# Kernel optimization log

Measured on AMD Instinct MI355X. Metric: run time of the kernel, lower is better.

The kernel has to match this reference:

```python
import jax, jax.numpy as jnp
import numpy as np
from jax import lax

B, C, N, T, K = 16, 64, 512, 64, 3
EPS = 1e-5


def _bn(x, g, b):
    # training-mode BatchNorm2d over (B, H=N, W=T) per channel
    m = jnp.mean(x, axis=(0, 2, 3), keepdims=True)
    v = jnp.var(x, axis=(0, 2, 3), keepdims=True)
    return (x - m) * lax.rsqrt(v + EPS) * g[None, :, None, None] + b[None, :, None, None]


def _conv(x, w, b, pad):
    y = lax.conv_general_dilated(x, w, (1, 1), ((0, 0), pad),
                                 dimension_numbers=('NCHW', 'OIHW', 'NCHW'))
    return y + b[None, :, None, None]


def setup_inputs() -> dict:
    key = jax.random.key(0)
    ks = jax.random.split(key, 8)
    xav = lambda k, sh, fi, fo: jax.random.normal(k, sh, jnp.float32) * np.sqrt(2.0 / (fi + fo))
    return {
        'x': jax.random.normal(ks[0], (B, C, N, T), jnp.float32),
        'adj_mx': jax.random.normal(ks[1], (K, N, N), jnp.float32) / np.sqrt(N),
        'cheb_w': xav(ks[2], (K, C, C), C, C),
        'cheb_b': jnp.zeros((C,), jnp.float32),
        'w1': xav(ks[3], (C, C, 1, 3), 3 * C, 3 * C),
        'b1': jnp.zeros((C,), jnp.float32),
        'g1': jnp.ones((C,), jnp.float32),
        'be1': jnp.zeros((C,), jnp.float32),
        'w2': xav(ks[4], (C, C, 1, 3), 3 * C, 3 * C),
        'b2': jnp.zeros((C,), jnp.float32),
        'g2': jnp.ones((C,), jnp.float32),
        'be2': jnp.zeros((C,), jnp.float32),
        'gate_w': xav(ks[5], (C, 2 * C, 1, 1), 2 * C, C),
        'gate_b': jnp.zeros((C,), jnp.float32),
        'res_w': xav(ks[6], (C, C, 1, 1), C, C),
        'res_b': jnp.zeros((C,), jnp.float32),
        'g3': jnp.ones((C,), jnp.float32),
        'be3': jnp.zeros((C,), jnp.float32),
    }


def _forward(x, adj_mx, cheb_w, cheb_b, w1, b1, g1, be1, w2, b2, g2, be2,
             gate_w, gate_b, res_w, res_b, g3, be3):
    # ChebFilterBlock: out[b,o,n,t] = sum_{k,i,m} x[b,i,m,t] adj[k,m,n] W[k,i,o] + bias
    spatial = jnp.einsum('bimt,kmn,kio->bont', x, adj_mx, cheb_w) \
              + cheb_b[None, :, None, None]
    # temporal branch: two (1,3) convs with BN+ReLU
    t = jax.nn.relu(_bn(_conv(x, w1, b1, (1, 1)), g1, be1))
    t = jax.nn.relu(_bn(_conv(t, w2, b2, (1, 1)), g2, be2))
    # gated fusion
    comb = jnp.concatenate([spatial, t], axis=1)
    gate = jax.nn.sigmoid(_conv(comb, gate_w, gate_b, (0, 0)))
    res = _conv(x, res_w, res_b, (0, 0))
    out = gate * spatial + (1.0 - gate) * t + res
    return _bn(out, g3, be3)


def reference(x, adj_mx, cheb_w, cheb_b, w1, b1, g1, be1, w2, b2, g2, be2,
              gate_w, gate_b, res_w, res_b, g3, be3):
    return _forward(x, adj_mx, cheb_w, cheb_b, w1, b1, g1, be1, w2, b2, g2, be2,
                    gate_w, gate_b, res_w, res_b, g3, be3)
```

## Files before the change

### kernel.cpp

```cpp
#include <hip/hip_runtime.h>
#include <hip/hip_bf16.h>
#include <cstdint>

#define BB 16
#define CC 64
#define NN 512
#define TT 64
#define KCH 3
#define PP (BB*NN*TT)
#define EPSB 1e-5f

typedef __bf16 bf16;
typedef __bf16 bf16x8 __attribute__((ext_vector_type(8)));
typedef __bf16 bf16x4 __attribute__((ext_vector_type(4)));
typedef float  f32x4  __attribute__((ext_vector_type(4)));

#define MFMA16(A,Bv,Cv) __builtin_amdgcn_mfma_f32_16x16x32_bf16((A),(Bv),(Cv),0,0,0)

__device__ __forceinline__ void gload_lds16(const bf16* g, bf16* l){
  __builtin_amdgcn_global_load_lds(
      (const __attribute__((address_space(1))) void*)g,
      (__attribute__((address_space(3))) void*)l, 16, 0, 0);
}

__global__ __launch_bounds__(256) void k_adjT(const float* __restrict__ adj,
                                              bf16* __restrict__ adjb){
  int idx = blockIdx.x*256 + threadIdx.x;
  int m = idx & 511, n = (idx >> 9) & 511, k = idx >> 18;
  adjb[idx] = (bf16)adj[((size_t)(k*512 + m))*512 + n];
}

__global__ __launch_bounds__(256) void k_wprep(const float* __restrict__ w1,
    const float* __restrict__ w2, const float* __restrict__ cw,
    const float* __restrict__ gw, const float* __restrict__ rw,
    bf16* __restrict__ w1p, bf16* __restrict__ w2p, bf16* __restrict__ cp,
    bf16* __restrict__ gp, bf16* __restrict__ rp){
  int tid = threadIdx.x;
  for (int e = tid; e < 6*2048; e += 256){
    int j = e&7, lane = (e>>3)&63, cf = (e>>9)&3, ks = e>>11;
    int k = ks*32 + (lane>>4)*8 + j, col = cf*16 + (lane&15);
    int kk = k >> 6, i = k & 63;
    w1p[e] = (bf16)w1[(col*64 + i)*3 + kk];
    w2p[e] = (bf16)w2[(col*64 + i)*3 + kk];
    cp[e]  = (bf16)cw[((size_t)kk*64 + i)*64 + col];
  }
  for (int e = tid; e < 4*2048; e += 256){
    int j = e&7, lane = (e>>3)&63, cf = (e>>9)&3, ks = e>>11;
    int k = ks*32 + (lane>>4)*8 + j, col = cf*16 + (lane&15);
    gp[e] = (bf16)gw[col*128 + k];
  }
  for (int e = tid; e < 2*2048; e += 256){
    int j = e&7, lane = (e>>3)&63, cf = (e>>9)&3, ks = e>>11;
    int k = ks*32 + (lane>>4)*8 + j, col = cf*16 + (lane&15);
    rp[e] = (bf16)rw[col*64 + k];
  }
}

__global__ __launch_bounds__(256) void k_xlb(const float* __restrict__ x,
                                             bf16* __restrict__ xlb){
  __shared__ float tile[64][65];
  int bn = blockIdx.x; int b = bn >> 9, n = bn & 511;
  int tid = threadIdx.x;
  const float* xp = x + ((size_t)(b*64)*512 + n)*64;
  for (int p = 0; p < 4; ++p){
    int q = p*256 + tid;
    int i = q >> 4, tc = (q & 15)*4;
    float4 v = *reinterpret_cast<const float4*>(xp + (size_t)i*512*64 + tc);
    tile[i][tc+0] = v.x; tile[i][tc+1] = v.y; tile[i][tc+2] = v.z; tile[i][tc+3] = v.w;
  }
  __syncthreads();
  bf16* op = xlb + (size_t)bn*4096;
  for (int p = 0; p < 2; ++p){
    int v8 = p*256 + tid;
    int t = v8 >> 3, ic = (v8 & 7)*8;
    bf16x8 o;
    #pragma unroll
    for (int e = 0; e < 8; ++e) o[e] = (bf16)tile[ic+e][t];
    *reinterpret_cast<bf16x8*>(op + t*64 + ic) = o;
  }
}

__global__ __launch_bounds__(256) void k_xmt(const float* __restrict__ x,
                                             bf16* __restrict__ xmt){
  __shared__ bf16 T[32768];
  int bid = blockIdx.x;
  int b = bid >> 6, i0 = ((bid >> 3) & 7)*8, m0 = (bid & 7)*64;
  int tid = threadIdx.x;
  #pragma unroll 4
  for (int it = 0; it < 32; ++it){
    int flat = it*256 + tid;
    int t4 = flat & 15, m = (flat >> 4) & 63, i = flat >> 10;
    float4 v = *reinterpret_cast<const float4*>(
        x + ((size_t)((b*64 + i0 + i)*512) + (m0 + m))*64 + t4*4);
    int im = i*64 + m;
    int slot = t4 ^ ((m ^ i) & 15);
    bf16x4 pk; pk[0] = (bf16)v.x; pk[1] = (bf16)v.y; pk[2] = (bf16)v.z; pk[3] = (bf16)v.w;
    *reinterpret_cast<bf16x4*>(&T[im*64 + slot*4]) = pk;
  }
  __syncthreads();
  #pragma unroll 4
  for (int it = 0; it < 16; ++it){
    int flat = it*256 + tid;
    int mc = flat & 7, i = (flat >> 3) & 7, t = flat >> 6;
    bf16x8 o;
    #pragma unroll
    for (int e = 0; e < 8; ++e){
      int m = mc*8 + e;
      int slot = (t >> 2) ^ ((m ^ i) & 15);
      o[e] = T[(i*64 + m)*64 + slot*4 + (t & 3)];
    }
    *reinterpret_cast<bf16x8*>(
        &xmt[((size_t)((b*64 + t)*64) + i0 + i)*512 + m0 + mc*8]) = o;
  }
}

__global__ __launch_bounds__(256,4) void k_conv(const bf16* __restrict__ in,
    const bf16* __restrict__ wp, bf16* __restrict__ outp, float* __restrict__ part,
    const float* __restrict__ sc, const float* __restrict__ sh){
  int tid = threadIdx.x, w = tid >> 6, l = tid & 63, l15 = l & 15, lg = l >> 4;
  int blk = blockIdx.x;
  size_t rowbase = (size_t)blk * 64;
  const bf16* xr = in + rowbase * 64;
  int t = w*16 + l15;
  f32x4 acc[4] = {};
  #pragma unroll
  for (int ks = 0; ks < 6; ++ks){
    int dt = ks >> 1, kh = ks & 1;
    int ts = t + dt - 1;
    bf16x8 a = {};
    if (ts >= 0 && ts < 64){
      a = *reinterpret_cast<const bf16x8*>(xr + ts*64 + kh*32 + lg*8);
      if (sc){
        int i0 = kh*32 + lg*8;
        #pragma unroll
        for (int e = 0; e < 8; ++e){
          float f = (float)a[e]*sc[i0+e] + sh[i0+e];
          a[e] = (bf16)fmaxf(f, 0.f);
        }
      }
    }
    #pragma unroll
    for (int cf = 0; cf < 4; ++cf){
      bf16x8 bfr = *reinterpret_cast<const bf16x8*>(wp + ((ks*4 + cf)*64 + l)*8);
      acc[cf] = MFMA16(a, bfr, acc[cf]);
    }
  }
  __shared__ float ssum[4][4][16], ssq[4][4][16];
  #pragma unroll
  for (int cf = 0; cf < 4; ++cf){
    int o = cf*16 + l15;
    float s = 0.f, q = 0.f;
    #pragma unroll
    for (int r = 0; r < 4; ++r){
      float vv = acc[cf][r];
      int to = w*16 + lg*4 + r;
      outp[(rowbase + to)*64 + o] = (bf16)vv;
      s += vv; q += vv*vv;
    }
    s += __shfl_xor(s, 16); s += __shfl_xor(s, 32);
    q += __shfl_xor(q, 16); q += __shfl_xor(q, 32);
    if (lg == 0){ ssum[w][cf][l15] = s; ssq[w][cf][l15] = q; }
  }
  __syncthreads();
  if (tid < 64){
    int cf = tid >> 4, c = tid & 15;
    float s = ssum[0][cf][c]+ssum[1][cf][c]+ssum[2][cf][c]+ssum[3][cf][c];
    float q = ssq[0][cf][c]+ssq[1][cf][c]+ssq[2][cf][c]+ssq[3][cf][c];
    part[(size_t)blk*128 + tid*2]     = s;
    part[(size_t)blk*128 + tid*2 + 1] = q;
  }
}

__global__ __launch_bounds__(256) void k_stats(const float* __restrict__ part, int nb,
    const float* __restrict__ g, const float* __restrict__ be,
    float* __restrict__ sc, float* __restrict__ sh){
  int c = blockIdx.x, tid = threadIdx.x;
  float s = 0.f, q = 0.f;
  for (int i = tid; i < nb; i += 256){
    s += part[(size_t)i*128 + c*2];
    q += part[(size_t)i*128 + c*2 + 1];
  }
  __shared__ float rs[256], rq[256];
  rs[tid] = s; rq[tid] = q; __syncthreads();
  for (int st = 128; st > 0; st >>= 1){
    if (tid < st){ rs[tid] += rs[tid+st]; rq[tid] += rq[tid+st]; }
    __syncthreads();
  }
  if (tid == 0){
    float cnt = (float)PP;
    float mean = rs[0]/cnt, var = rq[0]/cnt - mean*mean;
    float r = rsqrtf(var + EPSB);
    sc[c] = g[c]*r;
    sh[c] = be[c] - mean*g[c]*r;
  }
}

__global__ __launch_bounds__(512,4) void k_gemm1(const bf16* __restrict__ xmt,
    const bf16* __restrict__ adjb, const bf16* __restrict__ cp,
    const float* __restrict__ cb, bf16* __restrict__ spm){
  __shared__ bf16 As[2][4096];
  __shared__ bf16 Bs[2][4096];
  __shared__ bf16 VT[64*128];

  int tid = threadIdx.x, w = tid >> 6, l = tid & 63, l15 = l & 15, lg = l >> 4;
  int wr = w >> 2, wc = w & 3;

  int orig = blockIdx.x;
  int wg = (orig & 7) * 256 + (orig >> 3);
  int jt = wg >> 2, nt = wg & 3;
  int J0 = jt*128, N0 = nt*128;

  const bf16* aglob = xmt + (size_t)J0*512;
  const bf16* bbase = adjb + (size_t)N0*512;

  int sr = tid >> 2, sc = tid & 3;
  int scg = sc ^ (sr & 3) ^ ((sr >> 2) & 3);
  size_t soff = (size_t)sr*512 + scg*8;

  auto stage = [&](int t){
    int buf = t & 1;
    const bf16* bg = bbase + (size_t)(t >> 4)*(512*512);
    int m0 = (t & 15)*32;
    gload_lds16(aglob + soff + m0, &As[buf][tid*8]);
    gload_lds16(bg    + soff + m0, &Bs[buf][tid*8]);
  };

  int aoff[4], boff[2];
  #pragma unroll
  for (int rf = 0; rf < 4; ++rf){
    int row = wr*64 + rf*16 + l15;
    aoff[rf] = row*32 + ((lg ^ (row & 3) ^ ((row >> 2) & 3))*8);
  }
  #pragma unroll
  for (int cf = 0; cf < 2; ++cf){
    int row = wc*32 + cf*16 + l15;
    boff[cf] = row*32 + ((lg ^ (row & 3) ^ ((row >> 2) & 3))*8);
  }

  f32x4 acc[4][2] = {};
  f32x4 acc2[2][4] = {};

  stage(0);
  for (int t = 0; t < 48; ++t){
    if (t < 47){
      stage(t+1);
      asm volatile("s_waitcnt vmcnt(2)" ::: "memory");
    } else {
      asm volatile("s_waitcnt vmcnt(0)" ::: "memory");
    }
    __builtin_amdgcn_s_barrier();
    __builtin_amdgcn_sched_barrier(0);

    int buf = t & 1;
    bf16x8 a[4], bb[2];
    #pragma unroll
    for (int rf = 0; rf < 4; ++rf)
      a[rf] = *reinterpret_cast<const bf16x8*>(&As[buf][aoff[rf]]);
    #pragma unroll
    for (int cf = 0; cf < 2; ++cf)
      bb[cf] = *reinterpret_cast<const bf16x8*>(&Bs[buf][boff[cf]]);
    #pragma unroll
    for (int rf = 0; rf < 4; ++rf)
      #pragma unroll
      for (int cf = 0; cf < 2; ++cf)
        acc[rf][cf] = MFMA16(a[rf], bb[cf], acc[rf][cf]);

    asm volatile("s_waitcnt lgkmcnt(0)" ::: "memory");
    __builtin_amdgcn_sched_barrier(0);
    __builtin_amdgcn_s_barrier();

    if ((t & 15) == 15){
      int kk = t >> 4;
      #pragma unroll
      for (int h = 0; h < 2; ++h){
        if ((wc >> 1) == h){
          #pragma unroll
          for (int rf = 0; rf < 4; ++rf){
            int jb = wr*8 + rf*2 + (lg >> 1);
            #pragma unroll
            for (int cf = 0; cf < 2; ++cf){
              int nh = (wc & 1)*32 + cf*16 + l15;
              bf16x4 pk;
              #pragma unroll
              for (int r = 0; r < 4; ++r) pk[r] = (bf16)acc[rf][cf][r];
              *reinterpret_cast<bf16x4*>(
                  &VT[nh*128 + ((jb ^ (nh & 15)) << 3) + ((lg & 1) << 2)]) = pk;
            }
          }
        }
        asm volatile("s_waitcnt lgkmcnt(0)" ::: "memory");
        __builtin_amdgcn_sched_barrier(0);
        __builtin_amdgcn_s_barrier();

        #pragma unroll
        for (int ks2 = 0; ks2 < 2; ++ks2){
          bf16x8 bc[4];
          #pragma unroll
          for (int cf = 0; cf < 4; ++cf)
            bc[cf] = *reinterpret_cast<const bf16x8*>(
                cp + (((kk*2 + ks2)*4 + cf)*64 + l)*8);
          int nh = (w & 3)*16 + l15;
          int jb = (w >> 2)*8 + ks2*4 + lg;
          bf16x8 a2 = *reinterpret_cast<const bf16x8*>(
              &VT[nh*128 + ((jb ^ (nh & 15)) << 3)]);
          #pragma unroll
          for (int cf = 0; cf < 4; ++cf)
            acc2[h][cf] = MFMA16(a2, bc[cf], acc2[h][cf]);
        }
        asm volatile("s_waitcnt lgkmcnt(0)" ::: "memory");
        __builtin_amdgcn_sched_barrier(0);
        __builtin_amdgcn_s_barrier();
      }
      #pragma unroll
      for (int rf = 0; rf < 4; ++rf)
        #pragma unroll
        for (int cf = 0; cf < 2; ++cf)
          acc[rf][cf] = (f32x4){0.f, 0.f, 0.f, 0.f};
    }
  }

  bf16* SP = VT;
  float cbv[4];
  #pragma unroll
  for (int cf = 0; cf < 4; ++cf) cbv[cf] = cb[cf*16 + l15];
  int b = jt >> 5, t0 = (jt & 31)*2;
  #pragma unroll
  for (int hr = 0; hr < 2; ++hr){
    if ((w >> 2) == hr){
      #pragma unroll
      for (int h = 0; h < 2; ++h){
        int rowb = h*64 + (w & 3)*16 + lg*4;
        #pragma unroll
        for (int cf = 0; cf < 4; ++cf){
          int o = cf*16 + l15;
          #pragma unroll
          for (int r = 0; r < 4; ++r)
            SP[(rowb + r)*64 + o] = (bf16)(acc2[h][cf][r] + cbv[cf]);
        }
      }
    }
    __syncthreads();
    #pragma unroll
    for (int q = 0; q < 2; ++q){
      int flat = q*512 + tid;
      int n = flat >> 3, oc = (flat & 7)*8;
      bf16x8 vv = *reinterpret_cast<const bf16x8*>(&SP[n*64 + oc]);
      *reinterpret_cast<bf16x8*>(
          &spm[(((size_t)b*512 + N0 + n)*64 + (t0 + hr))*64 + oc]) = vv;
    }
    __syncthreads();
  }
}

__global__ __launch_bounds__(256,4) void k_fusion(const bf16* __restrict__ spm,
    const bf16* __restrict__ t2, const bf16* __restrict__ xlb,
    const bf16* __restrict__ gp, const bf16* __restrict__ rp,
    const float* __restrict__ sc2, const float* __restrict__ sh2,
    const float* __restrict__ gateb, bf16* __restrict__ pre,
    float* __restrict__ part){
  int tid = threadIdx.x, w = tid >> 6, l = tid & 63, l15 = l & 15, lg = l >> 4;
  int blk = blockIdx.x;
  int b = blk >> 9, n = blk & 511;
  size_t rowbase = (size_t)blk * 64;
  int t = w*16 + l15;
  f32x4 ag[4] = {}, ar[4] = {};
  #pragma unroll
  for (int ks = 0; ks < 4; ++ks){
    bf16x8 a;
    if (ks < 2){
      a = *reinterpret_cast<const bf16x8*>(spm + (rowbase + t)*64 + ks*32 + lg*8);
    } else {
      int i0 = (ks-2)*32 + lg*8;
      bf16x8 raw = *reinterpret_cast<const bf16x8*>(t2 + (rowbase + t)*64 + i0);
      #pragma unroll
      for (int e = 0; e < 8; ++e){
        float f = (float)raw[e]*sc2[i0+e] + sh2[i0+e];
        a[e] = (bf16)fmaxf(f, 0.f);
      }
    }
    #pragma unroll
    for (int cf = 0; cf < 4; ++cf){
      bf16x8 bfr = *reinterpret_cast<const bf16x8*>(gp + ((ks*4 + cf)*64 + l)*8);
      ag[cf] = MFMA16(a, bfr, ag[cf]);
    }
  }
  #pragma unroll
  for (int ks = 0; ks < 2; ++ks){
    bf16x8 a = *reinterpret_cast<const bf16x8*>(xlb + (rowbase + t)*64 + ks*32 + lg*8);
    #pragma unroll
    for (int cf = 0; cf < 4; ++cf){
      bf16x8 bfr = *reinterpret_cast<const bf16x8*>(rp + ((ks*4 + cf)*64 + l)*8);
      ar[cf] = MFMA16(a, bfr, ar[cf]);
    }
  }
  __shared__ float ssum[4][4][16], ssq[4][4][16];
  int tb = w*16 + lg*4;
  #pragma unroll
  for (int cf = 0; cf < 4; ++cf){
    int o = cf*16 + l15;
    float gb = gateb[o], sco = sc2[o], sho = sh2[o];
    float s = 0.f, q = 0.f;
    bf16x4 ov;
    #pragma unroll
    for (int r = 0; r < 4; ++r){
      size_t row = rowbase + tb + r;
      float z = ag[cf][r] + gb;
      float g = 1.f/(1.f + __expf(-z));
      float spv = (float)spm[row*64 + o];
      float tv  = (float)t2[row*64 + o];
      tv = fmaxf(tv*sco + sho, 0.f);
      float val = g*spv + (1.f - g)*tv + ar[cf][r];
      ov[r] = (bf16)val;
      s += val; q += val*val;
    }
    *reinterpret_cast<bf16x4*>(pre + (((size_t)b*64 + o)*512 + n)*64 + tb) = ov;
    s += __shfl_xor(s, 16); s += __shfl_xor(s, 32);
    q += __shfl_xor(q, 16); q += __shfl_xor(q, 32);
    if (lg == 0){ ssum[w][cf][l15] = s; ssq[w][cf][l15] = q; }
  }
  __syncthreads();
  if (tid < 64){
    int cf = tid >> 4, c = tid & 15;
    float s = ssum[0][cf][c]+ssum[1][cf][c]+ssum[2][cf][c]+ssum[3][cf][c];
    float q = ssq[0][cf][c]+ssq[1][cf][c]+ssq[2][cf][c]+ssq[3][cf][c];
    part[(size_t)blk*128 + tid*2]     = s;
    part[(size_t)blk*128 + tid*2 + 1] = q;
  }
}

__global__ __launch_bounds__(256) void k_bn3(const bf16* __restrict__ pre,
    float* __restrict__ out,
    const float* __restrict__ sc, const float* __restrict__ sh){
  size_t total8 = (size_t)BB*CC*NN*TT/8;
  for (size_t i8 = (size_t)blockIdx.x*256 + threadIdx.x; i8 < total8;
       i8 += (size_t)gridDim.x*256){
    bf16x8 v = reinterpret_cast<const bf16x8*>(pre)[i8];
    int o = (int)(i8 >> 12) & 63;
    float a = sc[o], bsh = sh[o];
    float4 r0, r1;
    r0.x = (float)v[0]*a + bsh; r0.y = (float)v[1]*a + bsh;
    r0.z = (float)v[2]*a + bsh; r0.w = (float)v[3]*a + bsh;
    r1.x = (float)v[4]*a + bsh; r1.y = (float)v[5]*a + bsh;
    r1.z = (float)v[6]*a + bsh; r1.w = (float)v[7]*a + bsh;
    reinterpret_cast<float4*>(out)[i8*2]     = r0;
    reinterpret_cast<float4*>(out)[i8*2 + 1] = r1;
  }
}

extern "C" void kernel_launch(void* const* d_in, const int* in_sizes, int n_in,
                              void* d_out, int out_size, void* d_ws, size_t ws_size,
                              hipStream_t stream){
  (void)in_sizes; (void)n_in; (void)out_size; (void)ws_size;
  const float* x   = (const float*)d_in[0];
  const float* adj = (const float*)d_in[1];
  const float* cw  = (const float*)d_in[2];
  const float* cb  = (const float*)d_in[3];
  const float* w1  = (const float*)d_in[4];
  const float* g1  = (const float*)d_in[6];
  const float* be1 = (const float*)d_in[7];
  const float* w2  = (const float*)d_in[8];
  const float* g2  = (const float*)d_in[10];
  const float* be2 = (const float*)d_in[11];
  const float* gw  = (const float*)d_in[12];
  const float* gb  = (const float*)d_in[13];
  const float* rw  = (const float*)d_in[14];
  const float* g3  = (const float*)d_in[16];
  const float* be3 = (const float*)d_in[17];
  float* out = (float*)d_out;

  char* ws = (char*)d_ws;
  size_t off = 0;
  auto alloc = [&](size_t bytes)->char*{
    char* p = ws + off; off += (bytes + 255) & ~(size_t)255; return p;
  };
  bf16* xlb  = (bf16*)alloc((size_t)PP*64*2);
  bf16* xmt  = (bf16*)alloc((size_t)PP*64*2);
  bf16* t1   = (bf16*)alloc((size_t)PP*64*2);
  bf16* t2   = (bf16*)alloc((size_t)PP*64*2);
  bf16* spm  = t1;
  bf16* pre  = xmt;
  bf16* adjb = (bf16*)alloc((size_t)KCH*512*512*2);
  bf16* w1p  = (bf16*)alloc(6*2048*2);
  bf16* w2p  = (bf16*)alloc(6*2048*2);
  bf16* cp   = (bf16*)alloc(6*2048*2);
  bf16* gp   = (bf16*)alloc(4*2048*2);
  bf16* rp   = (bf16*)alloc(2*2048*2);
  float* part = (float*)alloc((size_t)8192*128*4);
  float* s1sc = (float*)alloc(256); float* s1sh = (float*)alloc(256);
  float* s2sc = (float*)alloc(256); float* s2sh = (float*)alloc(256);
  float* s3sc = (float*)alloc(256); float* s3sh = (float*)alloc(256);

  k_adjT <<<dim3(3072), dim3(256), 0, stream>>>(adj, adjb);
  k_wprep<<<dim3(1),    dim3(256), 0, stream>>>(w1, w2, cw, gw, rw, w1p, w2p, cp, gp, rp);
  k_xlb  <<<dim3(8192), dim3(256), 0, stream>>>(x, xlb);
  k_xmt  <<<dim3(1024), dim3(256), 0, stream>>>(x, xmt);

  k_conv <<<dim3(8192), dim3(256), 0, stream>>>(xlb, w1p, t1, part, nullptr, nullptr);
  k_stats<<<dim3(64),   dim3(256), 0, stream>>>(part, 8192, g1, be1, s1sc, s1sh);
  k_conv <<<dim3(8192), dim3(256), 0, stream>>>(t1, w2p, t2, part, s1sc, s1sh);
  k_stats<<<dim3(64),   dim3(256), 0, stream>>>(part, 8192, g2, be2, s2sc, s2sh);

  k_gemm1<<<dim3(2048), dim3(512), 0, stream>>>(xmt, adjb, cp, cb, spm);

  k_fusion<<<dim3(8192), dim3(256), 0, stream>>>(spm, t2, xlb, gp, rp,
                                                 s2sc, s2sh, gb, pre, part);
  k_stats<<<dim3(64),   dim3(256), 0, stream>>>(part, 8192, g3, be3, s3sc, s3sh);
  k_bn3  <<<dim3(2048), dim3(256), 0, stream>>>(pre, out, s3sc, s3sh);
}
```

Baseline: 609.2 us.

## Merge prep kernels, fuse x transposes, triple-buffer gemm1 and drop VT barriers

Merges the adjacency transpose and weight packing into one parallel prep kernel, and fuses the two x layout conversions into a single kernel that reads x once from an LDS tile, with a new swizzle. In the adjacency GEMM it moves from double to triple buffering with a deeper prefetch. It also enlarges the VT scratch so all waves write their partial tile at once, which removes the serialized halves and their extra barriers in the Chebyshev weight stage and in the output write. The cost is more shared memory per block, which may lower occupancy of gemm1.

```diff
diff --git a/kernel.cpp b/kernel.cpp
--- a/kernel.cpp
+++ b/kernel.cpp
@@ -23,79 +23,56 @@
       (__attribute__((address_space(3))) void*)l, 16, 0, 0);
 }
 
-__global__ __launch_bounds__(256) void k_adjT(const float* __restrict__ adj,
-                                              bf16* __restrict__ adjb){
-  int idx = blockIdx.x*256 + threadIdx.x;
-  int m = idx & 511, n = (idx >> 9) & 511, k = idx >> 18;
-  adjb[idx] = (bf16)adj[((size_t)(k*512 + m))*512 + n];
-}
-
-__global__ __launch_bounds__(256) void k_wprep(const float* __restrict__ w1,
-    const float* __restrict__ w2, const float* __restrict__ cw,
-    const float* __restrict__ gw, const float* __restrict__ rw,
+__global__ __launch_bounds__(256) void k_prep(const float* __restrict__ adj,
+    const float* __restrict__ w1, const float* __restrict__ w2,
+    const float* __restrict__ cw, const float* __restrict__ gw,
+    const float* __restrict__ rw, bf16* __restrict__ adjb,
     bf16* __restrict__ w1p, bf16* __restrict__ w2p, bf16* __restrict__ cp,
     bf16* __restrict__ gp, bf16* __restrict__ rp){
-  int tid = threadIdx.x;
-  for (int e = tid; e < 6*2048; e += 256){
+  int blk = blockIdx.x, tid = threadIdx.x;
+  if (blk < 3072){
+    int idx = blk*256 + tid;
+    int m = idx & 511, n = (idx >> 9) & 511, k = idx >> 18;
+    adjb[idx] = (bf16)adj[((size_t)(k*512 + m))*512 + n];
+    return;
+  }
+  int e0 = (blk - 3072)*256 + tid;
+  if (e0 < 12288){
+    int e = e0;
     int j = e&7, lane = (e>>3)&63, cf = (e>>9)&3, ks = e>>11;
     int k = ks*32 + (lane>>4)*8 + j, col = cf*16 + (lane&15);
     int kk = k >> 6, i = k & 63;
     w1p[e] = (bf16)w1[(col*64 + i)*3 + kk];
     w2p[e] = (bf16)w2[(col*64 + i)*3 + kk];
     cp[e]  = (bf16)cw[((size_t)kk*64 + i)*64 + col];
-  }
-  for (int e = tid; e < 4*2048; e += 256){
+  } else if (e0 < 20480){
+    int e = e0 - 12288;
     int j = e&7, lane = (e>>3)&63, cf = (e>>9)&3, ks = e>>11;
     int k = ks*32 + (lane>>4)*8 + j, col = cf*16 + (lane&15);
     gp[e] = (bf16)gw[col*128 + k];
-  }
-  for (int e = tid; e < 2*2048; e += 256){
+  } else {
+    int e = e0 - 20480;
     int j = e&7, lane = (e>>3)&63, cf = (e>>9)&3, ks = e>>11;
     int k = ks*32 + (lane>>4)*8 + j, col = cf*16 + (lane&15);
     rp[e] = (bf16)rw[col*64 + k];
   }
 }
 
-__global__ __launch_bounds__(256) void k_xlb(const float* __restrict__ x,
-                                             bf16* __restrict__ xlb){
-  __shared__ float tile[64][65];
-  int bn = blockIdx.x; int b = bn >> 9, n = bn & 511;
-  int tid = threadIdx.x;
-  const float* xp = x + ((size_t)(b*64)*512 + n)*64;
-  for (int p = 0; p < 4; ++p){
-    int q = p*256 + tid;
-    int i = q >> 4, tc = (q & 15)*4;
-    float4 v = *reinterpret_cast<const float4*>(xp + (size_t)i*512*64 + tc);
-    tile[i][tc+0] = v.x; tile[i][tc+1] = v.y; tile[i][tc+2] = v.z; tile[i][tc+3] = v.w;
-  }
-  __syncthreads();
-  bf16* op = xlb + (size_t)bn*4096;
-  for (int p = 0; p < 2; ++p){
-    int v8 = p*256 + tid;
-    int t = v8 >> 3, ic = (v8 & 7)*8;
-    bf16x8 o;
-    #pragma unroll
-    for (int e = 0; e < 8; ++e) o[e] = (bf16)tile[ic+e][t];
-    *reinterpret_cast<bf16x8*>(op + t*64 + ic) = o;
-  }
-}
-
-__global__ __launch_bounds__(256) void k_xmt(const float* __restrict__ x,
-                                             bf16* __restrict__ xmt){
+__global__ __launch_bounds__(256) void k_xprep(const float* __restrict__ x,
+    bf16* __restrict__ xlb, bf16* __restrict__ xmt){
   __shared__ bf16 T[32768];
   int bid = blockIdx.x;
-  int b = bid >> 6, i0 = ((bid >> 3) & 7)*8, m0 = (bid & 7)*64;
+  int b = bid >> 6, i0 = ((bid >> 3) & 7)*8, n0 = (bid & 7)*64;
   int tid = threadIdx.x;
   #pragma unroll 4
   for (int it = 0; it < 32; ++it){
     int flat = it*256 + tid;
-    int t4 = flat & 15, m = (flat >> 4) & 63, i = flat >> 10;
+    int t4 = flat & 15, n = (flat >> 4) & 63, i = flat >> 10;
     float4 v = *reinterpret_cast<const float4*>(
-        x + ((size_t)((b*64 + i0 + i)*512) + (m0 + m))*64 + t4*4);
-    int im = i*64 + m;
-    int slot = t4 ^ ((m ^ i) & 15);
-    bf16x4 pk; pk[0] = (bf16)v.x; pk[1] = (bf16)v.y; pk[2] = (bf16)v.z; pk[3] = (bf16)v.w;
-    *reinterpret_cast<bf16x4*>(&T[im*64 + slot*4]) = pk;
+        x + ((size_t)((b*64 + i0 + i)*512) + (n0 + n))*64 + t4*4);
+    int s = t4 ^ ((n + 2*i) & 15);
+    bf16x4 pk; pk[0]=(bf16)v.x; pk[1]=(bf16)v.y; pk[2]=(bf16)v.z; pk[3]=(bf16)v.w;
+    *reinterpret_cast<bf16x4*>(&T[(i*64 + n)*64 + s*4]) = pk;
   }
   __syncthreads();
   #pragma unroll 4
@@ -106,11 +83,24 @@
     #pragma unroll
     for (int e = 0; e < 8; ++e){
       int m = mc*8 + e;
-      int slot = (t >> 2) ^ ((m ^ i) & 15);
-      o[e] = T[(i*64 + m)*64 + slot*4 + (t & 3)];
+      int s = (t >> 2) ^ ((m + 2*i) & 15);
+      o[e] = T[(i*64 + m)*64 + s*4 + (t & 3)];
     }
     *reinterpret_cast<bf16x8*>(
-        &xmt[((size_t)((b*64 + t)*64) + i0 + i)*512 + m0 + mc*8]) = o;
+        &xmt[((size_t)((b*64 + t)*64) + i0 + i)*512 + n0 + mc*8]) = o;
+  }
+  #pragma unroll 4
+  for (int it = 0; it < 16; ++it){
+    int flat = it*256 + tid;
+    int t = flat & 63, n = flat >> 6;
+    bf16x8 o;
+    #pragma unroll
+    for (int e = 0; e < 8; ++e){
+      int s = (t >> 2) ^ ((n + 2*e) & 15);
+      o[e] = T[(e*64 + n)*64 + s*4 + (t & 3)];
+    }
+    *reinterpret_cast<bf16x8*>(
+        &xlb[(((size_t)b*512 + n0 + n)*64 + t)*64 + i0]) = o;
   }
 }
 
@@ -198,9 +188,9 @@
 __global__ __launch_bounds__(512,4) void k_gemm1(const bf16* __restrict__ xmt,
     const bf16* __restrict__ adjb, const bf16* __restrict__ cp,
     const float* __restrict__ cb, bf16* __restrict__ spm){
-  __shared__ bf16 As[2][4096];
-  __shared__ bf16 Bs[2][4096];
-  __shared__ bf16 VT[64*128];
+  __shared__ bf16 As[3][4096];
+  __shared__ bf16 Bs[3][4096];
+  __shared__ bf16 VT[128*128];
 
   int tid = threadIdx.x, w = tid >> 6, l = tid & 63, l15 = l & 15, lg = l >> 4;
   int wr = w >> 2, wc = w & 3;
@@ -218,7 +208,7 @@
   size_t soff = (size_t)sr*512 + scg*8;
 
   auto stage = [&](int t){
-    int buf = t & 1;
+    int buf = t % 3;
     const bf16* bg = bbase + (size_t)(t >> 4)*(512*512);
     int m0 = (t & 15)*32;
     gload_lds16(aglob + soff + m0, &As[buf][tid*8]);
@@ -240,10 +230,12 @@
   f32x4 acc[4][2] = {};
   f32x4 acc2[2][4] = {};
 
-  stage(0);
+  stage(0); stage(1);
   for (int t = 0; t < 48; ++t){
-    if (t < 47){
-      stage(t+1);
+    if (t < 46){
+      stage(t+2);
+      asm volatile("s_waitcnt vmcnt(4)" ::: "memory");
+    } else if (t == 46){
       asm volatile("s_waitcnt vmcnt(2)" ::: "memory");
     } else {
       asm volatile("s_waitcnt vmcnt(0)" ::: "memory");
@@ -251,7 +243,7 @@
     __builtin_amdgcn_s_barrier();
     __builtin_amdgcn_sched_barrier(0);
 
-    int buf = t & 1;
+    int buf = t % 3;
     bf16x8 a[4], bb[2];
     #pragma unroll
     for (int rf = 0; rf < 4; ++rf)
@@ -272,34 +264,33 @@
     if ((t & 15) == 15){
       int kk = t >> 4;
       #pragma unroll
-      for (int h = 0; h < 2; ++h){
-        if ((wc >> 1) == h){
+      for (int rf = 0; rf < 4; ++rf){
+        int jb = wr*8 + rf*2 + (lg >> 1);
+        #pragma unroll
+        for (int cf = 0; cf < 2; ++cf){
+          int nh = wc*32 + cf*16 + l15;
+          bf16x4 pk;
           #pragma unroll
-          for (int rf = 0; rf < 4; ++rf){
-            int jb = wr*8 + rf*2 + (lg >> 1);
-            #pragma unroll
-            for (int cf = 0; cf < 2; ++cf){
-              int nh = (wc & 1)*32 + cf*16 + l15;
-              bf16x4 pk;
-              #pragma unroll
-              for (int r = 0; r < 4; ++r) pk[r] = (bf16)acc[rf][cf][r];
-              *reinterpret_cast<bf16x4*>(
-                  &VT[nh*128 + ((jb ^ (nh & 15)) << 3) + ((lg & 1) << 2)]) = pk;
-            }
-          }
+          for (int r = 0; r < 4; ++r) pk[r] = (bf16)acc[rf][cf][r];
+          *reinterpret_cast<bf16x4*>(
+              &VT[nh*128 + ((jb ^ (nh & 15)) << 3) + ((lg & 1) << 2)]) = pk;
+          acc[rf][cf] = (f32x4){0.f, 0.f, 0.f, 0.f};
         }
-        asm volatile("s_waitcnt lgkmcnt(0)" ::: "memory");
-        __builtin_amdgcn_sched_barrier(0);
-        __builtin_amdgcn_s_barrier();
-
+      }
+      asm volatile("s_waitcnt lgkmcnt(0)" ::: "memory");
+      __builtin_amdgcn_sched_barrier(0);
+      __builtin_amdgcn_s_barrier();
+
+      #pragma unroll
+      for (int ks2 = 0; ks2 < 2; ++ks2){
+        bf16x8 bc[4];
         #pragma unroll
-        for (int ks2 = 0; ks2 < 2; ++ks2){
-          bf16x8 bc[4];
-          #pragma unroll
-          for (int cf = 0; cf < 4; ++cf)
-            bc[cf] = *reinterpret_cast<const bf16x8*>(
-                cp + (((kk*2 + ks2)*4 + cf)*64 + l)*8);
-          int nh = (w & 3)*16 + l15;
+        for (int cf = 0; cf < 4; ++cf)
+          bc[cf] = *reinterpret_cast<const bf16x8*>(
+              cp + (((kk*2 + ks2)*4 + cf)*64 + l)*8);
+        #pragma unroll
+        for (int h = 0; h < 2; ++h){
+          int nh = h*64 + (w & 3)*16 + l15;
           int jb = (w >> 2)*8 + ks2*4 + lg;
           bf16x8 a2 = *reinterpret_cast<const bf16x8*>(
               &VT[nh*128 + ((jb ^ (nh & 15)) << 3)]);
@@ -307,48 +298,36 @@
           for (int cf = 0; cf < 4; ++cf)
             acc2[h][cf] = MFMA16(a2, bc[cf], acc2[h][cf]);
         }
-        asm volatile("s_waitcnt lgkmcnt(0)" ::: "memory");
-        __builtin_amdgcn_sched_barrier(0);
-        __builtin_amdgcn_s_barrier();
       }
-      #pragma unroll
-      for (int rf = 0; rf < 4; ++rf)
-        #pragma unroll
-        for (int cf = 0; cf < 2; ++cf)
-          acc[rf][cf] = (f32x4){0.f, 0.f, 0.f, 0.f};
-    }
-  }
-
+    }
+  }
+
+  __syncthreads();
   bf16* SP = VT;
   float cbv[4];
   #pragma unroll
   for (int cf = 0; cf < 4; ++cf) cbv[cf] = cb[cf*16 + l15];
   int b = jt >> 5, t0 = (jt & 31)*2;
   #pragma unroll
-  for (int hr = 0; hr < 2; ++hr){
-    if ((w >> 2) == hr){
+  for (int h = 0; h < 2; ++h){
+    int rowb = (w >> 2)*128 + h*64 + (w & 3)*16 + lg*4;
+    #pragma unroll
+    for (int cf = 0; cf < 4; ++cf){
+      int o = cf*16 + l15;
       #pragma unroll
-      for (int h = 0; h < 2; ++h){
-        int rowb = h*64 + (w & 3)*16 + lg*4;
-        #pragma unroll
-        for (int cf = 0; cf < 4; ++cf){
-          int o = cf*16 + l15;
-          #pragma unroll
-          for (int r = 0; r < 4; ++r)
-            SP[(rowb + r)*64 + o] = (bf16)(acc2[h][cf][r] + cbv[cf]);
-        }
-      }
-    }
-    __syncthreads();
-    #pragma unroll
-    for (int q = 0; q < 2; ++q){
-      int flat = q*512 + tid;
-      int n = flat >> 3, oc = (flat & 7)*8;
-      bf16x8 vv = *reinterpret_cast<const bf16x8*>(&SP[n*64 + oc]);
-      *reinterpret_cast<bf16x8*>(
-          &spm[(((size_t)b*512 + N0 + n)*64 + (t0 + hr))*64 + oc]) = vv;
-    }
-    __syncthreads();
+      for (int r = 0; r < 4; ++r)
+        SP[(rowb + r)*64 + o] = (bf16)(acc2[h][cf][r] + cbv[cf]);
+    }
+  }
+  __syncthreads();
+  #pragma unroll
+  for (int q = 0; q < 4; ++q){
+    int flat = q*512 + tid;
+    int row = flat >> 3, oc = (flat & 7)*8;
+    int tl = row >> 7, n = row & 127;
+    bf16x8 vv = *reinterpret_cast<const bf16x8*>(&SP[row*64 + oc]);
+    *reinterpret_cast<bf16x8*>(
+        &spm[(((size_t)b*512 + N0 + n)*64 + (t0 + tl))*64 + oc]) = vv;
   }
 }
 
@@ -490,10 +469,9 @@
   float* s2sc = (float*)alloc(256); float* s2sh = (float*)alloc(256);
   float* s3sc = (float*)alloc(256); float* s3sh = (float*)alloc(256);
 
-  k_adjT <<<dim3(3072), dim3(256), 0, stream>>>(adj, adjb);
-  k_wprep<<<dim3(1),    dim3(256), 0, stream>>>(w1, w2, cw, gw, rw, w1p, w2p, cp, gp, rp);
-  k_xlb  <<<dim3(8192), dim3(256), 0, stream>>>(x, xlb);
-  k_xmt  <<<dim3(1024), dim3(256), 0, stream>>>(x, xmt);
+  k_prep <<<dim3(3168), dim3(256), 0, stream>>>(adj, w1, w2, cw, gw, rw,
+                                                adjb, w1p, w2p, cp, gp, rp);
+  k_xprep<<<dim3(1024), dim3(256), 0, stream>>>(x, xlb, xmt);
 
   k_conv <<<dim3(8192), dim3(256), 0, stream>>>(xlb, w1p, t1, part, nullptr, nullptr);
   k_stats<<<dim3(64),   dim3(256), 0, stream>>>(part, 8192, g1, be1, s1sc, s1sh);
```

Result: faster. 548.4 us (-10.0%).
